# Optimization experiments

Measured on AMD Instinct MI355X. Metric: run time of the kernel, lower is better.

## Reference

```python
import jax, jax.numpy as jnp
import numpy as np
import math

H = 8
D_MODEL = 32
D_HEAD = 4
FACTOR = 5
EPS = 1e-5

DATANUM = 1024
B = 512            # outer batch; becomes attention sequence length
C = 32
L = DATANUM // 8   # 128; becomes attention batch
U = min(FACTOR * int(math.ceil(math.log(B))), B)  # 35 (U_part == u since L_Q == L_K == B)


def setup_inputs() -> dict:
    key = jax.random.key(0)
    ks = jax.random.split(key, 16)
    s = 0.05
    return {
        'x': jax.random.normal(ks[0], (B, C, L), jnp.float32),
        'Wq': jax.random.normal(ks[1], (D_MODEL, D_MODEL), jnp.float32) * s,
        'bq': jnp.zeros((D_MODEL,), jnp.float32),
        'Wk': jax.random.normal(ks[2], (D_MODEL, D_MODEL), jnp.float32) * s,
        'bk': jnp.zeros((D_MODEL,), jnp.float32),
        'Wv': jax.random.normal(ks[3], (D_MODEL, D_MODEL), jnp.float32) * s,
        'bv': jnp.zeros((D_MODEL,), jnp.float32),
        'Wo': jax.random.normal(ks[4], (D_MODEL, D_MODEL), jnp.float32) * s,
        'bo': jnp.zeros((D_MODEL,), jnp.float32),
        'bn1_gamma': jnp.ones((C,), jnp.float32),
        'bn1_beta': jnp.zeros((C,), jnp.float32),
        'bn1_mean': jnp.zeros((C,), jnp.float32),
        'bn1_var': jnp.ones((C,), jnp.float32),
        'W1': jax.random.normal(ks[5], (DATANUM * 8, DATANUM * 4), jnp.float32) * 0.01,
        'b1': jnp.zeros((DATANUM * 8,), jnp.float32),
        'W2': jax.random.normal(ks[6], (DATANUM * 4, DATANUM * 8), jnp.float32) * 0.01,
        'b2': jnp.zeros((DATANUM * 4,), jnp.float32),
        'bn2_gamma': jnp.ones((C,), jnp.float32),
        'bn2_beta': jnp.zeros((C,), jnp.float32),
        'bn2_mean': jnp.zeros((C,), jnp.float32),
        'bn2_var': jnp.ones((C,), jnp.float32),
        'index_sample': jax.random.randint(ks[7], (B, U), 0, B, jnp.int64),
    }


def _bn(x, gamma, beta, mean, var):
    # eval-mode BatchNorm1d over channel dim of (batch, C, length)
    inv = jax.lax.rsqrt(var + EPS)
    return (x - mean[None, :, None]) * (inv * gamma)[None, :, None] + beta[None, :, None]


def _prob_attention(Q, K, V, index_sample):
    # Q,K,V: (Ba, H, Lq, D) self-attention, Lq == Lk. Informer ProbAttention, mask_flag=True.
    Ba, Hh, Lq, D = Q.shape
    u = index_sample.shape[1]
    # sparsity measurement on sampled keys
    K_sample = K[:, :, index_sample, :]                       # (Ba,H,Lq,U,D)
    QK_sample = jnp.einsum('bhld,bhlud->bhlu', Q, K_sample)
    M = QK_sample.max(axis=-1) - QK_sample.sum(axis=-1) / Lq  # (Ba,H,Lq)
    _, M_top = jax.lax.top_k(M, u)                            # (Ba,H,u) selected queries
    Q_reduce = jnp.take_along_axis(Q, M_top[..., None], axis=2)  # (Ba,H,u,D)
    scores = jnp.einsum('bhud,bhkd->bhuk', Q_reduce, K) / jnp.sqrt(jnp.float32(D))
    # ProbMask: causal w.r.t. the selected query's original position
    causal = jnp.arange(Lq)[None, None, None, :] > M_top[..., None]
    scores = jnp.where(causal, -jnp.inf, scores)
    attn = jax.nn.softmax(scores, axis=-1)
    upd = jnp.einsum('bhuk,bhkd->bhud', attn, V)              # (Ba,H,u,D)
    context = jnp.cumsum(V, axis=2)                           # initial context (mask_flag=True)
    b_idx = jnp.arange(Ba)[:, None, None]
    h_idx = jnp.arange(Hh)[None, :, None]
    context = context.at[b_idx, h_idx, M_top].set(upd)
    return context


def reference(x, Wq, bq, Wk, bk, Wv, bv, Wo, bo,
              bn1_gamma, bn1_beta, bn1_mean, bn1_var,
              W1, b1, W2, b2,
              bn2_gamma, bn2_beta, bn2_mean, bn2_var,
              index_sample):
    Bsz, Cc, Ll = x.shape
    res1 = x
    xa = jnp.transpose(x, (2, 0, 1))                          # (L, B, 32): attn batch=L, seq=B

    def heads(t):
        return jnp.transpose(t.reshape(Ll, Bsz, H, D_HEAD), (0, 2, 1, 3))

    Q = heads(xa @ Wq.T + bq)
    K = heads(xa @ Wk.T + bk)
    V = heads(xa @ Wv.T + bv)
    ctx = _prob_attention(Q, K, V, index_sample)              # (L,H,B,D)
    out = jnp.transpose(ctx, (0, 2, 1, 3)).reshape(Ll, Bsz, D_MODEL)
    out = out @ Wo.T + bo
    xh = jax.nn.relu(out)                                     # dropout = identity (eval)
    xh = jnp.transpose(xh, (1, 2, 0))                         # (B,32,L)
    xh = _bn(xh + res1, bn1_gamma, bn1_beta, bn1_mean, bn1_var)
    res2 = xh
    f = xh.reshape(Bsz, Cc * Ll)
    f = jax.nn.relu(f @ W1.T + b1)
    f = jax.nn.relu(f @ W2.T + b2)
    f = f.reshape(Bsz, Cc, Ll)
    return _bn(f + res2, bn2_gamma, bn2_beta, bn2_mean, bn2_var)
```

## Files before the change

### kernel.cpp

```cpp
#include <hip/hip_runtime.h>
#include <stdint.h>

#define EPSF 1e-5f
#define NEG_INF (-1e30f)

typedef float f32x4 __attribute__((ext_vector_type(4)));
typedef __bf16 bf16x8 __attribute__((ext_vector_type(8)));
typedef unsigned short u16x8 __attribute__((ext_vector_type(8)));
typedef _Float16 h16;
typedef _Float16 h16x8 __attribute__((ext_vector_type(8)));

typedef __attribute__((address_space(3))) unsigned char* as3_ptr;
typedef const __attribute__((address_space(1))) unsigned char* as1_ptr;

__device__ __forceinline__ void async16(const void* g, void* l) {
  __builtin_amdgcn_global_load_lds((as1_ptr)g, (as3_ptr)l, 16, 0, 0);
}

__device__ __forceinline__ unsigned short f2bf(float f) {
  union { float f; unsigned int u; } v; v.f = f;
  unsigned int r = v.u + 0x7FFFu + ((v.u >> 16) & 1u);
  return (unsigned short)(r >> 16);
}
__device__ __forceinline__ unsigned short f2bf_fast(float f) {
  union { float f; unsigned int u; } v; v.f = f;
  return (unsigned short)((v.u + 0x8000u) >> 16);
}

__global__ __launch_bounds__(256) void transpose_k(const float* __restrict__ src,
                                                   float* __restrict__ dst, int R, int C) {
  __shared__ float tl[32][33];
  int tx = threadIdx.x & 31, ty = threadIdx.x >> 5;
  int c0 = blockIdx.x * 32, r0 = blockIdx.y * 32;
#pragma unroll
  for (int i = 0; i < 4; i++)
    tl[ty + i * 8][tx] = src[(size_t)(r0 + ty + i * 8) * C + c0 + tx];
  __syncthreads();
#pragma unroll
  for (int i = 0; i < 4; i++)
    dst[(size_t)(c0 + ty + i * 8) * R + r0 + tx] = tl[tx][ty + i * 8];
}

__global__ __launch_bounds__(256) void qkv_k(const float* __restrict__ xT,
    const float* __restrict__ Wq, const float* __restrict__ bq,
    const float* __restrict__ Wk, const float* __restrict__ bk,
    const float* __restrict__ Wv, const float* __restrict__ bv,
    float* __restrict__ Q, float* __restrict__ Kq, float* __restrict__ Vq) {
  __shared__ float xs[64 * 33];
  __shared__ float wq[32 * 33], wk[32 * 33], wvs[32 * 33];
  __shared__ float bqs[32], bks[32], bvs[32];
  int tid = threadIdx.x;
  int a = blockIdx.x;
  int tbase = blockIdx.y * 256;
#pragma unroll
  for (int i = 0; i < 4; i++) {
    int e = i * 256 + tid; int r = e >> 5, c = e & 31;
    wq[r * 33 + c] = Wq[e]; wk[r * 33 + c] = Wk[e]; wvs[r * 33 + c] = Wv[e];
  }
  if (tid < 32) { bqs[tid] = bq[tid]; bks[tid] = bk[tid]; bvs[tid] = bv[tid]; }
  int tl = tid & 63, rg = tid >> 6;
  for (int ch = 0; ch < 4; ch++) {
    __syncthreads();
#pragma unroll
    for (int i = 0; i < 8; i++) {
      int e = i * 256 + tid; int r = e >> 5, c = e & 31;
      xs[r * 33 + c] = xT[(size_t)a * 16384 + (size_t)(tbase + ch * 64) * 32 + e];
    }
    __syncthreads();
    float qa[8], ka[8], va[8];
#pragma unroll
    for (int r8 = 0; r8 < 8; r8++) {
      int r = rg * 8 + r8; qa[r8] = bqs[r]; ka[r8] = bks[r]; va[r8] = bvs[r];
    }
    for (int c = 0; c < 32; c++) {
      float xv = xs[tl * 33 + c];
#pragma unroll
      for (int r8 = 0; r8 < 8; r8++) {
        int r = rg * 8 + r8;
        qa[r8] += xv * wq[r * 33 + c];
        ka[r8] += xv * wk[r * 33 + c];
        va[r8] += xv * wvs[r * 33 + c];
      }
    }
    int t = tbase + ch * 64 + tl;
#pragma unroll
    for (int r8 = 0; r8 < 8; r8++) {
      int r = rg * 8 + r8;
      size_t o = (size_t)a * 16384 + (size_t)r * 512 + t;
      Q[o] = qa[r8]; Kq[o] = ka[r8]; Vq[o] = va[r8];
    }
  }
}

__global__ __launch_bounds__(512) void topattn_k(const float* __restrict__ Q,
    const float* __restrict__ Kq, const float* __restrict__ Vq,
    const int* __restrict__ idxs, float* __restrict__ Ctx, int U) {
  __shared__ float Ks[2048];
  __shared__ float Vs[2048];
  __shared__ float Ml[512];
  __shared__ int mt[64];
  __shared__ float Qr[64][4];
  __shared__ float upd[64][4];
  int bh = blockIdx.x;
  int tid = threadIdx.x, lane = tid & 63, wv = tid >> 6;
  size_t base = (size_t)bh * 2048;
#pragma unroll
  for (int i = 0; i < 4; i++) {
    Ks[i * 512 + tid] = Kq[base + i * 512 + tid];
    Vs[i * 512 + tid] = Vq[base + i * 512 + tid];
  }
  float q0 = Q[base + tid], q1 = Q[base + 512 + tid];
  float q2 = Q[base + 1024 + tid], q3 = Q[base + 1536 + tid];
  __syncthreads();
  float mx = NEG_INF, sm = 0.f;
  for (int u = 0; u < U; u++) {
    int it = idxs[tid * U + u];
    it = min(max(it, 0), 511);
    float s = q0 * Ks[it] + q1 * Ks[512 + it] + q2 * Ks[1024 + it] + q3 * Ks[1536 + it];
    mx = fmaxf(mx, s); sm += s;
  }
  Ml[tid] = mx - sm * (1.f / 512.f);
  __syncthreads();
  float mi = Ml[tid];
  int rank = 0;
  for (int j0 = 0; j0 < 512; j0 += 4) {
    float4 m4 = *(const float4*)(Ml + j0);
    rank += (m4.x > mi) || (m4.x == mi && (j0 + 0) < tid);
    rank += (m4.y > mi) || (m4.y == mi && (j0 + 1) < tid);
    rank += (m4.z > mi) || (m4.z == mi && (j0 + 2) < tid);
    rank += (m4.w > mi) || (m4.w == mi && (j0 + 3) < tid);
  }
  if (rank < U) mt[rank] = tid;
  __syncthreads();
  if (tid < 4 * U) { int u = tid >> 2, d = tid & 3; Qr[u][d] = Q[base + d * 512 + mt[u]]; }
  __syncthreads();
  for (int u = wv; u < U; u += 8) {
    int mrow = mt[u];
    float p0q = Qr[u][0], p1q = Qr[u][1], p2q = Qr[u][2], p3q = Qr[u][3];
    float sv[8]; float lmax = NEG_INF;
#pragma unroll
    for (int jj = 0; jj < 8; jj++) {
      int k = jj * 64 + lane;
      float s = NEG_INF;
      if (k <= mrow)
        s = 0.5f * (p0q * Ks[k] + p1q * Ks[512 + k] + p2q * Ks[1024 + k] + p3q * Ks[1536 + k]);
      sv[jj] = s; lmax = fmaxf(lmax, s);
    }
#pragma unroll
    for (int off = 32; off; off >>= 1) lmax = fmaxf(lmax, __shfl_xor(lmax, off));
    float ls = 0.f, p0 = 0.f, p1 = 0.f, p2 = 0.f, p3 = 0.f;
#pragma unroll
    for (int jj = 0; jj < 8; jj++) {
      int k = jj * 64 + lane;
      if (k <= mrow) {
        float p = __expf(sv[jj] - lmax);
        ls += p; p0 += p * Vs[k]; p1 += p * Vs[512 + k];
        p2 += p * Vs[1024 + k]; p3 += p * Vs[1536 + k];
      }
    }
#pragma unroll
    for (int off = 32; off; off >>= 1) {
      ls += __shfl_xor(ls, off); p0 += __shfl_xor(p0, off); p1 += __shfl_xor(p1, off);
      p2 += __shfl_xor(p2, off); p3 += __shfl_xor(p3, off);
    }
    if (lane == 0) {
      float inv = 1.f / ls;
      upd[u][0] = p0 * inv; upd[u][1] = p1 * inv; upd[u][2] = p2 * inv; upd[u][3] = p3 * inv;
    }
  }
  __syncthreads();
  if (wv < 4) {
    float v[8];
    int b0 = wv * 512 + lane * 8;
#pragma unroll
    for (int q = 0; q < 8; q++) v[q] = Vs[b0 + q];
#pragma unroll
    for (int q = 1; q < 8; q++) v[q] += v[q - 1];
    float x = v[7];
    for (int off = 1; off < 64; off <<= 1) {
      float y = __shfl_up(x, off);
      if (lane >= off) x += y;
    }
    float excl = x - v[7];
#pragma unroll
    for (int q = 0; q < 8; q++) Vs[b0 + q] = v[q] + excl;
  }
  __syncthreads();
  if (tid < 4 * U) { int u = tid >> 2, d = tid & 3; Vs[d * 512 + mt[u]] = upd[u][d]; }
  __syncthreads();
#pragma unroll
  for (int i = 0; i < 4; i++) Ctx[base + i * 512 + tid] = Vs[i * 512 + tid];
}

__global__ __launch_bounds__(256) void oproj_k(const float* __restrict__ Ctx,
    const float* __restrict__ Wo, const float* __restrict__ bo, float* __restrict__ Y) {
  __shared__ float cs[32 * 256];
  __shared__ float wo[32 * 33];
  __shared__ float bos[32];
  int tid = threadIdx.x;
  int a = blockIdx.x, t0 = blockIdx.y * 256;
#pragma unroll
  for (int i = 0; i < 4; i++) {
    int e = i * 256 + tid; int r = e >> 5, c = e & 31;
    wo[r * 33 + c] = Wo[e];
  }
  if (tid < 32) bos[tid] = bo[tid];
#pragma unroll
  for (int i = 0; i < 32; i++) {
    int e = i * 256 + tid; int row = e >> 8, col = e & 255;
    cs[e] = Ctx[(size_t)a * 16384 + (size_t)row * 512 + t0 + col];
  }
  __syncthreads();
  int rl = tid & 31, tw = tid >> 5;
  for (int ti = 0; ti < 32; ti++) {
    int t = ti * 8 + tw;
    float acc = bos[rl];
#pragma unroll
    for (int rp = 0; rp < 32; rp++) acc += cs[rp * 256 + t] * wo[rl * 33 + rp];
    Y[(size_t)a * 16384 + (size_t)(t0 + t) * 32 + rl] = acc;
  }
}

__global__ __launch_bounds__(256) void bn1t_k(const float* __restrict__ Y,
    const float* __restrict__ x, const float* __restrict__ g1, const float* __restrict__ be1,
    const float* __restrict__ me1, const float* __restrict__ va1,
    float* __restrict__ Xh, unsigned short* __restrict__ Fb) {
  __shared__ float tl[32][33];
  int tx = threadIdx.x & 31, ty = threadIdx.x >> 5;
  int c0 = blockIdx.x * 32;
  int r0 = blockIdx.y * 32;
#pragma unroll
  for (int i = 0; i < 4; i++)
    tl[ty + i * 8][tx] = Y[(size_t)(r0 + ty + i * 8) * 16384 + c0 + tx];
  __syncthreads();
#pragma unroll
  for (int i = 0; i < 4; i++) {
    int m = c0 + ty + i * 8;
    int a = r0 + tx;
    float v = tl[tx][ty + i * 8];
    int ch = m & 31;
    size_t oi = (size_t)m * 128 + a;
    float val = fmaxf(v, 0.f) + x[oi];
    float s = g1[ch] * rsqrtf(va1[ch] + EPSF);
    float res = (val - me1[ch]) * s + be1[ch];
    Xh[oi] = res;
    Fb[oi] = f2bf(res);
  }
}

__global__ __launch_bounds__(256) void wcvt_k(const float* __restrict__ W,
    unsigned short* __restrict__ Wb, int n4) {
  int stride = gridDim.x * 256;
  for (int idx = blockIdx.x * 256 + threadIdx.x; idx < n4; idx += stride) {
    float4 w = ((const float4*)W)[idx];
    ushort4 o;
    o.x = f2bf(w.x); o.y = f2bf(w.y); o.z = f2bf(w.z); o.w = f2bf(w.w);
    ((ushort4*)Wb)[idx] = o;
  }
}

__global__ __launch_bounds__(256, 3) void gemm_bf(
    const unsigned short* __restrict__ A, const unsigned short* __restrict__ B,
    int K, int N, int MT, int NPX, int SPLITK, h16* __restrict__ P, int M) {
  __shared__ unsigned char lds[16384];
  int tid = threadIdx.x;
  int lane = tid & 63, wv = tid >> 6;
  int wm = wv >> 1, wn = wv & 1;
  int lin = blockIdx.x;
  int xcd = lin & 7, slot = lin >> 3;
  int tilesPerSp = MT * NPX;
  int sp = slot / tilesPerSp;
  int rem = slot % tilesPerSp;
  int mt = rem % MT;
  int nt = xcd * NPX + rem / MT;
  int mtile0 = mt * 128, ntile0 = nt * 128;
  int m0 = mtile0 + wm * 64, n0 = ntile0 + wn * 64;
  int frow = lane & 15, q = lane >> 4;

  int nk = K / (32 * SPLITK);
  int kbase = sp * (K / SPLITK);

  f32x4 acc[4][4];
#pragma unroll
  for (int i = 0; i < 4; i++)
#pragma unroll
    for (int j = 0; j < 4; j++) { f32x4 z = {0.f, 0.f, 0.f, 0.f}; acc[i][j] = z; }

  for (int k = 0; k < nk; k++) {
    int ks = kbase + k * 32;
#pragma unroll
    for (int i = 0; i < 2; i++) {
      int e = i * 256 + tid;
      int row = e >> 2;
      int g = (e & 3) ^ ((row >> 1) & 3);
      async16(A + (size_t)(mtile0 + row) * K + ks + g * 8, lds + i * 4096 + wv * 1024);
    }
#pragma unroll
    for (int i = 0; i < 2; i++) {
      int e = i * 256 + tid;
      int row = e >> 2;
      int g = (e & 3) ^ ((row >> 1) & 3);
      async16(B + (size_t)(ntile0 + row) * K + ks + g * 8,
              lds + 8192 + i * 4096 + wv * 1024);
    }
    __syncthreads();
    bf16x8 af[4], bfr[4];
#pragma unroll
    for (int i = 0; i < 4; i++) {
      int row = wm * 64 + i * 16 + frow;
      af[i] = *(const bf16x8*)(lds + row * 64 + ((q ^ ((row >> 1) & 3)) << 4));
    }
#pragma unroll
    for (int j = 0; j < 4; j++) {
      int row = wn * 64 + j * 16 + frow;
      bfr[j] = *(const bf16x8*)(lds + 8192 + row * 64 + ((q ^ ((row >> 1) & 3)) << 4));
    }
#pragma unroll
    for (int i = 0; i < 4; i++)
#pragma unroll
      for (int j = 0; j < 4; j++)
        acc[i][j] = __builtin_amdgcn_mfma_f32_16x16x32_bf16(af[i], bfr[j], acc[i][j], 0, 0, 0);
    __syncthreads();
  }

  h16* pb = P + (size_t)sp * M * N;
#pragma unroll
  for (int i = 0; i < 4; i++)
#pragma unroll
    for (int j = 0; j < 4; j++) {
      int n = n0 + j * 16 + frow;
      int mb = m0 + i * 16 + (q << 2);
#pragma unroll
      for (int r = 0; r < 4; r++)
        pb[(size_t)(mb + r) * N + n] = (h16)acc[i][j][r];
    }
}

template <int MI, int NJ, int EPI>
__global__ __launch_bounds__(256) void gemm_ps(
    const unsigned short* __restrict__ A, const float* __restrict__ Bw,
    const float* __restrict__ bias, int K, int N, int MT, int NPX, int SPLITK,
    h16* __restrict__ Pout, int M,
    unsigned short* __restrict__ Hout, const float* __restrict__ res2,
    const float* __restrict__ g2, const float* __restrict__ be2,
    const float* __restrict__ me2, const float* __restrict__ va2,
    float* __restrict__ Out) {
  constexpr int BM = MI * 32;
  constexpr int BN = NJ * 32;
  constexpr int ABYTES = BM * 32 * 2;
  constexpr int BBYTES = BN * 32 * 4;
  constexpr int SA = ABYTES / 4096;
  constexpr int SB = BBYTES / 4096;
  __shared__ unsigned char lds[ABYTES + BBYTES];
  int tid = threadIdx.x;
  int lane = tid & 63, wv = tid >> 6;
  int wm = wv >> 1, wn = wv & 1;
  int lin = blockIdx.x;
  int xcd = lin & 7, slot = lin >> 3;
  int tilesPerSp = MT * NPX;
  int sp = slot / tilesPerSp;
  int rem = slot % tilesPerSp;
  int mt = rem % MT;
  int nt = xcd * NPX + rem / MT;
  int m0 = mt * BM + wm * (BM / 2);
  int n0 = nt * BN + wn * (BN / 2);
  int frow = lane & 15, q = lane >> 4;
  int nk = K / (32 * SPLITK);
  int kbase = sp * (K / SPLITK);
  f32x4 acc[MI][NJ];
#pragma unroll
  for (int i = 0; i < MI; i++)
#pragma unroll
    for (int j = 0; j < NJ; j++) { f32x4 z = {0.f, 0.f, 0.f, 0.f}; acc[i][j] = z; }
  int mtile0 = mt * BM, ntile0 = nt * BN;
  for (int k = 0; k < nk; k++) {
    int ks = kbase + k * 32;
#pragma unroll
    for (int i = 0; i < SA; i++) {
      int e = i * 256 + tid;
      int row = e >> 2;
      int g = (e & 3) ^ ((row >> 1) & 3);
      async16(A + (size_t)(mtile0 + row) * K + ks + g * 8, lds + i * 4096 + wv * 1024);
    }
#pragma unroll
    for (int i = 0; i < SB; i++) {
      int e = i * 256 + tid;
      int row = e >> 3;
      int g = (e & 7) ^ (row & 7);
      async16(Bw + (size_t)(ntile0 + row) * K + ks + g * 4,
              lds + ABYTES + i * 4096 + wv * 1024);
    }
    __syncthreads();
    bf16x8 af[MI];
    bf16x8 bfr[NJ];
#pragma unroll
    for (int i = 0; i < MI; i++) {
      int row = wm * (BM / 2) + i * 16 + frow;
      af[i] = *(const bf16x8*)(lds + row * 64 + ((q ^ ((row >> 1) & 3)) << 4));
    }
#pragma unroll
    for (int j = 0; j < NJ; j++) {
      int row = wn * (BN / 2) + j * 16 + frow;
      const unsigned char* rb = lds + ABYTES + row * 128;
      int sw = row & 7;
      float4 w0 = *(const float4*)(rb + (((2 * q + 0) ^ sw) << 4));
      float4 w1 = *(const float4*)(rb + (((2 * q + 1) ^ sw) << 4));
      union { u16x8 u; bf16x8 b; } cv;
      cv.u[0] = f2bf_fast(w0.x); cv.u[1] = f2bf_fast(w0.y);
      cv.u[2] = f2bf_fast(w0.z); cv.u[3] = f2bf_fast(w0.w);
      cv.u[4] = f2bf_fast(w1.x); cv.u[5] = f2bf_fast(w1.y);
      cv.u[6] = f2bf_fast(w1.z); cv.u[7] = f2bf_fast(w1.w);
      bfr[j] = cv.b;
    }
#pragma unroll
    for (int i = 0; i < MI; i++)
#pragma unroll
      for (int j = 0; j < NJ; j++)
        acc[i][j] = __builtin_amdgcn_mfma_f32_16x16x32_bf16(af[i], bfr[j], acc[i][j], 0, 0, 0);
    __syncthreads();
  }
#pragma unroll
  for (int i = 0; i < MI; i++)
#pragma unroll
    for (int j = 0; j < NJ; j++) {
      int n = n0 + j * 16 + frow;
      int mb = m0 + i * 16 + (q << 2);
      if constexpr (EPI == 2) {
        h16* pb = Pout + (size_t)sp * M * N;
#pragma unroll
        for (int r = 0; r < 4; r++)
          pb[(size_t)(mb + r) * N + n] = (h16)acc[i][j][r];
      } else if constexpr (EPI == 0) {
        float bb = bias[n];
#pragma unroll
        for (int r = 0; r < 4; r++) {
          float v = fmaxf(acc[i][j][r] + bb, 0.f);
          Hout[(size_t)(mb + r) * N + n] = f2bf(v);
        }
      } else {
        float bb = bias[n];
        int ch = n >> 7;
        float s = g2[ch] * rsqrtf(va2[ch] + EPSF);
        float mu = me2[ch], bt = be2[ch];
#pragma unroll
        for (int r = 0; r < 4; r++) {
          float v = fmaxf(acc[i][j][r] + bb, 0.f);
          size_t oi = (size_t)(mb + r) * N + n;
          v += res2[oi];
          Out[oi] = (v - mu) * s + bt;
        }
      }
    }
}

template <int EPI>
__global__ __launch_bounds__(256) void redh_k(const h16* __restrict__ P, int SP,
    const float* __restrict__ bias, const float* __restrict__ Xh,
    const float* __restrict__ g2, const float* __restrict__ be2,
    const float* __restrict__ me2, const float* __restrict__ va2,
    unsigned short* __restrict__ H, float* __restrict__ Out, int N, int MN) {
  int idx = blockIdx.x * 256 + threadIdx.x;
  const h16x8* p = (const h16x8*)P;
  int mn8 = MN >> 3;
  h16x8 v0 = p[idx];
  float s[8];
#pragma unroll
  for (int e = 0; e < 8; e++) s[e] = (float)v0[e];
  for (int sp = 1; sp < SP; sp++) {
    h16x8 t = p[idx + (size_t)sp * mn8];
#pragma unroll
    for (int e = 0; e < 8; e++) s[e] += (float)t[e];
  }
  size_t off = (size_t)idx * 8;
  int n = (int)(off & (size_t)(N - 1));
  float4 b0 = *(const float4*)(bias + n);
  float4 b1 = *(const float4*)(bias + n + 4);
  float bb[8] = {b0.x, b0.y, b0.z, b0.w, b1.x, b1.y, b1.z, b1.w};
  if constexpr (EPI == 0) {
    u16x8 o;
#pragma unroll
    for (int e = 0; e < 8; e++) o[e] = f2bf(fmaxf(s[e] + bb[e], 0.f));
    *(u16x8*)(H + off) = o;
  } else {
    int ch = n >> 7;
    float sc = g2[ch] * rsqrtf(va2[ch] + EPSF);
    float mu = me2[ch], bt = be2[ch];
    float4 x0 = *(const float4*)(Xh + off);
    float4 x1 = *(const float4*)(Xh + off + 4);
    float xx[8] = {x0.x, x0.y, x0.z, x0.w, x1.x, x1.y, x1.z, x1.w};
    float oo[8];
#pragma unroll
    for (int e = 0; e < 8; e++)
      oo[e] = (fmaxf(s[e] + bb[e], 0.f) + xx[e] - mu) * sc + bt;
    float4 o0 = {oo[0], oo[1], oo[2], oo[3]};
    float4 o1 = {oo[4], oo[5], oo[6], oo[7]};
    *(float4*)(Out + off) = o0;
    *(float4*)(Out + off + 4) = o1;
  }
}

extern "C" void kernel_launch(void* const* d_in, const int* in_sizes, int n_in,
                              void* d_out, int out_size, void* d_ws, size_t ws_size,
                              hipStream_t stream) {
  const float* x  = (const float*)d_in[0];
  const float* Wq = (const float*)d_in[1];  const float* bq = (const float*)d_in[2];
  const float* Wk = (const float*)d_in[3];  const float* bk = (const float*)d_in[4];
  const float* Wv = (const float*)d_in[5];  const float* bv = (const float*)d_in[6];
  const float* Wo = (const float*)d_in[7];  const float* bo = (const float*)d_in[8];
  const float* g1 = (const float*)d_in[9];  const float* be1 = (const float*)d_in[10];
  const float* me1 = (const float*)d_in[11]; const float* va1 = (const float*)d_in[12];
  const float* W1 = (const float*)d_in[13]; const float* b1 = (const float*)d_in[14];
  const float* W2 = (const float*)d_in[15]; const float* b2 = (const float*)d_in[16];
  const float* g2 = (const float*)d_in[17]; const float* be2 = (const float*)d_in[18];
  const float* me2 = (const float*)d_in[19]; const float* va2 = (const float*)d_in[20];
  const int* idxs = (const int*)d_in[21];
  int U = in_sizes[21] / 512;
  float* out = (float*)d_out;

  char* ws = (char*)d_ws;
  float* QC = (float*)(ws);
  float* Kb = (float*)(ws + (8u << 20));
  float* Vb = (float*)(ws + (16u << 20));
  float* YT = (float*)(ws + (24u << 20));
  float* Xh = (float*)(ws + (32u << 20));
  unsigned short* Fb = (unsigned short*)Vb;
  unsigned short* Hb = (unsigned short*)Kb;
  unsigned short* Wb = (unsigned short*)(ws + (48u << 20));
  h16* PA = (h16*)(ws + (112u << 20));
  h16* P1 = (h16*)(ws + (48u << 20));
  h16* P2 = (h16*)(ws + (80u << 20));
  bool tierA = ws_size >= (size_t)176 * (1u << 20);
  bool tierB = !tierA && ws_size >= (size_t)112 * (1u << 20);

  dim3 b256(256);
  transpose_k<<<dim3(4, 512), b256, 0, stream>>>(x, YT, 16384, 128);
  qkv_k<<<dim3(128, 2), b256, 0, stream>>>(YT, Wq, bq, Wk, bk, Wv, bv, QC, Kb, Vb);
  topattn_k<<<dim3(1024), dim3(512), 0, stream>>>(QC, Kb, Vb, idxs, QC, U);
  oproj_k<<<dim3(128, 2), b256, 0, stream>>>(QC, Wo, bo, YT);
  bn1t_k<<<dim3(512, 4), b256, 0, stream>>>(YT, x, g1, be1, me1, va1, Xh, Fb);

  if (tierA) {
    wcvt_k<<<dim3(2048), b256, 0, stream>>>(W1, Wb, (8192 * 4096) / 4);
    gemm_bf<<<dim3(1024), b256, 0, stream>>>(Fb, Wb, 4096, 8192, 4, 8, 4, PA, 512);
    redh_k<0><<<dim3(2048), b256, 0, stream>>>(PA, 4, b1, nullptr, nullptr, nullptr,
                                               nullptr, nullptr, Hb, nullptr, 8192,
                                               512 * 8192);
    wcvt_k<<<dim3(2048), b256, 0, stream>>>(W2, Wb, (4096 * 8192) / 4);
    gemm_bf<<<dim3(1024), b256, 0, stream>>>(Hb, Wb, 8192, 4096, 4, 4, 8, PA, 512);
    redh_k<1><<<dim3(1024), b256, 0, stream>>>(PA, 8, b2, Xh, g2, be2, me2, va2,
                                               nullptr, out, 4096, 512 * 4096);
  } else if (tierB) {
    gemm_ps<4, 2, 2><<<dim3(1024), b256, 0, stream>>>(
        Fb, W1, nullptr, 4096, 8192, 4, 16, 2, P1, 512,
        nullptr, nullptr, nullptr, nullptr, nullptr, nullptr, nullptr);
    redh_k<0><<<dim3(2048), b256, 0, stream>>>(P1, 2, b1, nullptr, nullptr, nullptr,
                                               nullptr, nullptr, Hb, nullptr, 8192,
                                               512 * 8192);
    gemm_ps<4, 2, 2><<<dim3(1024), b256, 0, stream>>>(
        Hb, W2, nullptr, 8192, 4096, 4, 8, 4, P2, 512,
        nullptr, nullptr, nullptr, nullptr, nullptr, nullptr, nullptr);
    redh_k<1><<<dim3(1024), b256, 0, stream>>>(P2, 4, b2, Xh, g2, be2, me2, va2,
                                               nullptr, out, 4096, 512 * 4096);
  } else {
    gemm_ps<4, 2, 0><<<dim3(512), b256, 0, stream>>>(
        Fb, W1, b1, 4096, 8192, 4, 16, 1, nullptr, 512,
        Hb, nullptr, nullptr, nullptr, nullptr, nullptr, nullptr);
    gemm_ps<4, 2, 1><<<dim3(256), b256, 0, stream>>>(
        Hb, W2, b2, 8192, 4096, 4, 8, 1, nullptr, 512,
        nullptr, Xh, g2, be2, me2, va2, out);
  }
}
```

Measured before the change: 534.3 us.

## Fold bf16 weight conversion into attention and GEMM kernels to hide it

Removes the standalone weight-conversion kernels. The W1 fp32-to-bf16 conversion now runs as a tail loop of the attention kernel, and W2's conversion runs as a tail loop of the first GEMM, writing to separate workspace buffers. The aim is to overlap that memory-bound conversion with latency-bound or compute-bound work and save launches. In exchange, the largest path now needs more workspace (240MB), so tierA may silently fall back to tierB when less is provided. The tail loops also lengthen those kernels.

```diff
diff --git a/kernel.cpp b/kernel.cpp
--- a/kernel.cpp
+++ b/kernel.cpp
@@ -94,7 +94,8 @@
 
 __global__ __launch_bounds__(512) void topattn_k(const float* __restrict__ Q,
     const float* __restrict__ Kq, const float* __restrict__ Vq,
-    const int* __restrict__ idxs, float* __restrict__ Ctx, int U) {
+    const int* __restrict__ idxs, float* __restrict__ Ctx, int U,
+    const float* __restrict__ Wsrc, unsigned short* __restrict__ Wdst, int wn4) {
   __shared__ float Ks[2048];
   __shared__ float Vs[2048];
   __shared__ float Ml[512];
@@ -190,6 +191,15 @@
   __syncthreads();
 #pragma unroll
   for (int i = 0; i < 4; i++) Ctx[base + i * 512 + tid] = Vs[i * 512 + tid];
+  if (Wsrc) {
+    int gstride = gridDim.x * 512;
+    for (int i = bh * 512 + tid; i < wn4; i += gstride) {
+      float4 w = ((const float4*)Wsrc)[i];
+      ushort4 o;
+      o.x = f2bf(w.x); o.y = f2bf(w.y); o.z = f2bf(w.z); o.w = f2bf(w.w);
+      ((ushort4*)Wdst)[i] = o;
+    }
+  }
 }
 
 __global__ __launch_bounds__(256) void oproj_k(const float* __restrict__ Ctx,
@@ -248,20 +258,10 @@
   }
 }
 
-__global__ __launch_bounds__(256) void wcvt_k(const float* __restrict__ W,
-    unsigned short* __restrict__ Wb, int n4) {
-  int stride = gridDim.x * 256;
-  for (int idx = blockIdx.x * 256 + threadIdx.x; idx < n4; idx += stride) {
-    float4 w = ((const float4*)W)[idx];
-    ushort4 o;
-    o.x = f2bf(w.x); o.y = f2bf(w.y); o.z = f2bf(w.z); o.w = f2bf(w.w);
-    ((ushort4*)Wb)[idx] = o;
-  }
-}
-
 __global__ __launch_bounds__(256, 3) void gemm_bf(
     const unsigned short* __restrict__ A, const unsigned short* __restrict__ B,
-    int K, int N, int MT, int NPX, int SPLITK, h16* __restrict__ P, int M) {
+    int K, int N, int MT, int NPX, int SPLITK, h16* __restrict__ P, int M,
+    const float* __restrict__ Wsrc, unsigned short* __restrict__ Wdst, int wn4) {
   __shared__ unsigned char lds[16384];
   int tid = threadIdx.x;
   int lane = tid & 63, wv = tid >> 6;
@@ -334,6 +334,15 @@
       for (int r = 0; r < 4; r++)
         pb[(size_t)(mb + r) * N + n] = (h16)acc[i][j][r];
     }
+  if (Wsrc) {
+    int gstride = gridDim.x * 256;
+    for (int i = lin * 256 + tid; i < wn4; i += gstride) {
+      float4 w = ((const float4*)Wsrc)[i];
+      ushort4 o;
+      o.x = f2bf(w.x); o.y = f2bf(w.y); o.z = f2bf(w.z); o.w = f2bf(w.w);
+      ((ushort4*)Wdst)[i] = o;
+    }
+  }
 }
 
 template <int MI, int NJ, int EPI>
@@ -525,28 +534,32 @@
   float* Xh = (float*)(ws + (32u << 20));
   unsigned short* Fb = (unsigned short*)Vb;
   unsigned short* Hb = (unsigned short*)Kb;
-  unsigned short* Wb = (unsigned short*)(ws + (48u << 20));
-  h16* PA = (h16*)(ws + (112u << 20));
+  unsigned short* Wb1 = (unsigned short*)(ws + (48u << 20));
+  unsigned short* Wb2 = (unsigned short*)(ws + (120u << 20));
+  h16* PA = (h16*)(ws + (192u << 20));
   h16* P1 = (h16*)(ws + (48u << 20));
   h16* P2 = (h16*)(ws + (80u << 20));
-  bool tierA = ws_size >= (size_t)176 * (1u << 20);
+  bool tierA = ws_size >= (size_t)240 * (1u << 20);
   bool tierB = !tierA && ws_size >= (size_t)112 * (1u << 20);
+
+  const int WN4 = (8192 * 4096) / 4;
 
   dim3 b256(256);
   transpose_k<<<dim3(4, 512), b256, 0, stream>>>(x, YT, 16384, 128);
   qkv_k<<<dim3(128, 2), b256, 0, stream>>>(YT, Wq, bq, Wk, bk, Wv, bv, QC, Kb, Vb);
-  topattn_k<<<dim3(1024), dim3(512), 0, stream>>>(QC, Kb, Vb, idxs, QC, U);
+  topattn_k<<<dim3(1024), dim3(512), 0, stream>>>(QC, Kb, Vb, idxs, QC, U,
+                                                  tierA ? W1 : nullptr, Wb1, WN4);
   oproj_k<<<dim3(128, 2), b256, 0, stream>>>(QC, Wo, bo, YT);
   bn1t_k<<<dim3(512, 4), b256, 0, stream>>>(YT, x, g1, be1, me1, va1, Xh, Fb);
 
   if (tierA) {
-    wcvt_k<<<dim3(2048), b256, 0, stream>>>(W1, Wb, (8192 * 4096) / 4);
-    gemm_bf<<<dim3(1024), b256, 0, stream>>>(Fb, Wb, 4096, 8192, 4, 8, 4, PA, 512);
+    gemm_bf<<<dim3(1024), b256, 0, stream>>>(Fb, Wb1, 4096, 8192, 4, 8, 4, PA, 512,
+                                             W2, Wb2, WN4);
     redh_k<0><<<dim3(2048), b256, 0, stream>>>(PA, 4, b1, nullptr, nullptr, nullptr,
                                                nullptr, nullptr, Hb, nullptr, 8192,
                                                512 * 8192);
-    wcvt_k<<<dim3(2048), b256, 0, stream>>>(W2, Wb, (4096 * 8192) / 4);
-    gemm_bf<<<dim3(1024), b256, 0, stream>>>(Hb, Wb, 8192, 4096, 4, 4, 8, PA, 512);
+    gemm_bf<<<dim3(1024), b256, 0, stream>>>(Hb, Wb2, 8192, 4096, 4, 4, 8, PA, 512,
+                                             nullptr, nullptr, 0);
     redh_k<1><<<dim3(1024), b256, 0, stream>>>(PA, 8, b2, Xh, g2, be2, me2, va2,
                                                nullptr, out, 4096, 512 * 4096);
   } else if (tierB) {
```

New measurement: 536.6 us. Within noise of the previous version (+0.4%).
